# Kernel optimization log

Hardware: AMD Instinct MI355X
Metric: run time of the kernel (lower is better)

## Reference

```python
import jax, jax.numpy as jnp
import numpy as np

N = 100000
IN_C = 256
HID = 128


def setup_inputs() -> dict:
    key = jax.random.key(0)
    ks = jax.random.split(key, 8)
    x = jax.random.normal(ks[0], (N, IN_C), dtype=jnp.float32)
    edge_index = jax.random.randint(ks[1], (2, 1600000), 0, N, dtype=jnp.int64)
    # GCNConv: lin (bias=False) + separate additive bias
    W1 = jax.random.normal(ks[2], (IN_C, HID), dtype=jnp.float32) / np.sqrt(IN_C)
    b1 = jnp.zeros((HID,), dtype=jnp.float32)
    W2 = jax.random.normal(ks[3], (HID, HID // 2), dtype=jnp.float32) / np.sqrt(HID)
    b2 = jnp.zeros((HID // 2,), dtype=jnp.float32)
    Wfc = jax.random.normal(ks[4], (HID // 2, 2), dtype=jnp.float32) / np.sqrt(HID // 2)
    bfc = jnp.zeros((2,), dtype=jnp.float32)
    return {"x": x, "edge_index": edge_index, "W1": W1, "b1": b1,
            "W2": W2, "b2": b2, "Wfc": Wfc, "bfc": bfc}


def _gcn_norm(edge_index, n):
    # add self-loops, symmetric normalization (PyG gcn_norm defaults)
    loop = jnp.arange(n, dtype=edge_index.dtype)
    src = jnp.concatenate([edge_index[0], loop])
    dst = jnp.concatenate([edge_index[1], loop])
    deg = jax.ops.segment_sum(jnp.ones_like(src, dtype=jnp.float32), dst,
                              num_segments=n)
    dinv = jnp.where(deg > 0, jax.lax.rsqrt(deg), 0.0)
    norm = dinv[src] * dinv[dst]  # [E + N]
    return src, dst, norm


def _gcn_conv(x, W, b, src, dst, norm, n):
    h = x @ W                       # [N, out] dense transform first
    msg = h[src] * norm[:, None]    # irregular gather, [E+N, out]
    out = jax.ops.segment_sum(msg, dst, num_segments=n)  # scatter-add
    return out + b


def reference(x, edge_index, W1, b1, W2, b2, Wfc, bfc):
    n = x.shape[0]
    src, dst, norm = _gcn_norm(edge_index, n)
    h = jax.nn.relu(_gcn_conv(x, W1, b1, src, dst, norm, n))
    # dropout is identity in eval mode
    h = jax.nn.relu(_gcn_conv(h, W2, b2, src, dst, norm, n))
    logits = h @ Wfc + bfc  # [N, 2]
    return jax.nn.log_softmax(logits, axis=1)
```

## Files before the change

kernel.cpp:

```cpp
#include <hip/hip_runtime.h>
#include <math.h>

#define IN_C 256
#define HID 128
#define H2  64
#define CAP 64
#define NBK 391
#define BSLAB 8192

typedef __attribute__((ext_vector_type(8))) short bf16x8;
typedef __attribute__((ext_vector_type(4))) float f32x4;

__device__ __forceinline__ unsigned short f2bf(float f) {
  union { float f; unsigned int u; } v; v.f = f;
  unsigned int r = v.u + 0x7FFFu + ((v.u >> 16) & 1u);
  return (unsigned short)(r >> 16);
}
__device__ __forceinline__ float bf_lo(unsigned int u) {
  union { unsigned int u; float f; } v; v.u = u << 16; return v.f;
}
__device__ __forceinline__ float bf_hi(unsigned int u) {
  union { unsigned int u; float f; } v; v.u = u & 0xffff0000u; return v.f;
}
__device__ __forceinline__ unsigned int pack_bf(float lo, float hi) {
  return (unsigned int)f2bf(lo) | ((unsigned int)f2bf(hi) << 16);
}
__device__ __forceinline__ void add8(float* a, uint4 u) {
  a[0] += bf_lo(u.x); a[1] += bf_hi(u.x);
  a[2] += bf_lo(u.y); a[3] += bf_hi(u.y);
  a[4] += bf_lo(u.z); a[5] += bf_hi(u.z);
  a[6] += bf_lo(u.w); a[7] += bf_hi(u.w);
}

__global__ void wcast_kernel(const float* __restrict__ W, unsigned short* __restrict__ Wt,
                             int K, int N) {
  int idx = blockIdx.x * 256 + threadIdx.x;
  if (idx < K * N) {
    int nn = idx / K, kk = idx % K;
    Wt[idx] = f2bf(W[kk * N + nn]);
  }
}

__global__ __launch_bounds__(256) void scatter_kernel(
    const int* __restrict__ src, const int* __restrict__ dstA, int E,
    int* __restrict__ bucketFill , unsigned int* __restrict__ packed) {
  __shared__ int cnt[NBK];
  __shared__ int base[NBK];
  int tid = threadIdx.x;
  for (int i = tid; i < NBK; i += 256) cnt[i] = 0;
  __syncthreads();
  int e0 = blockIdx.x * 2048;
  int bk[8], ls[8]; unsigned int sv[8]; bool ok[8];
#pragma unroll
  for (int j = 0; j < 8; ++j) {
    int e = e0 + j * 256 + tid;
    ok[j] = e < E;
    int d = ok[j] ? dstA[e] : 0;
    int s = ok[j] ? src[e] : 0;
    bk[j] = d >> 8;
    sv[j] = ((unsigned int)s << 8) | (unsigned int)(d & 255);
    ls[j] = ok[j] ? atomicAdd(&cnt[bk[j]], 1) : 0;
  }
  __syncthreads();
  for (int i = tid; i < NBK; i += 256)
    base[i] = cnt[i] ? atomicAdd(&bucketFill[i * 16], cnt[i]) : 0;
  __syncthreads();
#pragma unroll
  for (int j = 0; j < 8; ++j)
    if (ok[j]) {
      int pos = base[bk[j]] + ls[j];
      if (pos < BSLAB) packed[(size_t)bk[j] * BSLAB + pos] = sv[j];
    }
}

__global__ __launch_bounds__(256) void bucket_csr_kernel(
    const unsigned int* __restrict__ packed, const int* __restrict__ bucketFill,
    int* __restrict__ fill, float* __restrict__ dinv, int* __restrict__ col, int n) {
  __shared__ int lcnt[256];
  int b = blockIdx.x;
  int t = threadIdx.x;
  lcnt[t] = 0;
  __syncthreads();
  int m = bucketFill[b * 16];
  if (m > BSLAB) m = BSLAB;
  const unsigned int* pp = packed + (size_t)b * BSLAB;
  int node0 = b * 256;
  for (int i = t; i < m; i += 256) {
    unsigned int p = pp[i];
    int lo = p & 255;
    int slot = atomicAdd(&lcnt[lo], 1);
    if (slot < CAP) col[(size_t)(node0 + lo) * CAP + slot] = (int)(p >> 8);
  }
  __syncthreads();
  int node = node0 + t;
  if (node < n) {
    int c = lcnt[t];
    fill[node] = c;
    dinv[node] = rsqrtf((float)(c + 1));
  }
}

template <int K, int N, int BM, int WM, int WN, bool A_BF16, bool SCALE>
__device__ __forceinline__ void gemm_body(const void* __restrict__ Av,
                                          const unsigned short* __restrict__ Bt,
                                          const float* __restrict__ dinv,
                                          unsigned short* __restrict__ C, int M,
                                          int bidx, short* As, short* Bs) {
  constexpr int WTM = BM / WM;
  constexpr int WTN = N / WN;
  constexpr int MB = WTM / 16, NB = WTN / 16;
  constexpr int ACH = BM * 4 / 256;
  constexpr int BCH = N * 4 / 256;

  int tid = threadIdx.x;
  int lane = tid & 63, wid = tid >> 6;
  int ln15 = lane & 15, kg = lane >> 4;
  int wm = wid / WN, wn = wid % WN;
  int row0 = bidx * BM;

  f32x4 acc[MB][NB];
#pragma unroll
  for (int i = 0; i < MB; ++i)
#pragma unroll
    for (int j = 0; j < NB; ++j) acc[i][j] = (f32x4)0.0f;

  for (int k0 = 0; k0 < K; k0 += 32) {
#pragma unroll
    for (int p = 0; p < ACH; ++p) {
      int c = p * 256 + tid;
      int row = c >> 2, kc = c & 3;
      int grow = row0 + row;
      if (A_BF16) {
        const unsigned short* Ab = (const unsigned short*)Av;
        uint4 v = make_uint4(0, 0, 0, 0);
        if (grow < M) v = *reinterpret_cast<const uint4*>(&Ab[(size_t)grow * K + k0 + kc * 8]);
        *reinterpret_cast<uint4*>(&As[row * 40 + kc * 8]) = v;
      } else {
        const float* A = (const float*)Av;
        float4 v0 = make_float4(0.f, 0.f, 0.f, 0.f), v1 = v0;
        if (grow < M) {
          const float4* ap = reinterpret_cast<const float4*>(&A[(size_t)grow * K + k0 + kc * 8]);
          v0 = ap[0]; v1 = ap[1];
        }
        bf16x8 w;
        w[0] = (short)f2bf(v0.x); w[1] = (short)f2bf(v0.y);
        w[2] = (short)f2bf(v0.z); w[3] = (short)f2bf(v0.w);
        w[4] = (short)f2bf(v1.x); w[5] = (short)f2bf(v1.y);
        w[6] = (short)f2bf(v1.z); w[7] = (short)f2bf(v1.w);
        *reinterpret_cast<bf16x8*>(&As[row * 40 + kc * 8]) = w;
      }
    }
#pragma unroll
    for (int p = 0; p < BCH; ++p) {
      int c = p * 256 + tid;
      int nrow = c >> 2, kc = c & 3;
      *reinterpret_cast<uint4*>(&Bs[nrow * 40 + kc * 8]) =
          *reinterpret_cast<const uint4*>(&Bt[(size_t)nrow * K + k0 + kc * 8]);
    }
    __syncthreads();
    bf16x8 af[MB], bfr[NB];
#pragma unroll
    for (int mb = 0; mb < MB; ++mb)
      af[mb] = *reinterpret_cast<const bf16x8*>(&As[(wm * WTM + mb * 16 + ln15) * 40 + kg * 8]);
#pragma unroll
    for (int nb = 0; nb < NB; ++nb)
      bfr[nb] = *reinterpret_cast<const bf16x8*>(&Bs[(wn * WTN + nb * 16 + ln15) * 40 + kg * 8]);
#pragma unroll
    for (int mb = 0; mb < MB; ++mb)
#pragma unroll
      for (int nb = 0; nb < NB; ++nb)
        acc[mb][nb] = __builtin_amdgcn_mfma_f32_16x16x32_bf16(af[mb], bfr[nb], acc[mb][nb], 0, 0, 0);
    __syncthreads();
  }
#pragma unroll
  for (int mb = 0; mb < MB; ++mb)
#pragma unroll
    for (int nb = 0; nb < NB; ++nb) {
      int gcol = wn * WTN + nb * 16 + ln15;
#pragma unroll
      for (int q = 0; q < 4; ++q) {
        int grow = row0 + wm * WTM + mb * 16 + kg * 4 + q;
        if (grow < M) {
          float v = acc[mb][nb][q];
          if (SCALE) v *= dinv[grow];
          C[(size_t)grow * N + gcol] = f2bf(v);
        }
      }
    }
}

__global__ __launch_bounds__(256) void gemm1_kernel(const float* __restrict__ A,
                                                    const unsigned short* __restrict__ Bt,
                                                    const float* __restrict__ dinv,
                                                    unsigned short* __restrict__ C, int M) {
  __shared__ short smem[(64 + HID) * 40];
  gemm_body<IN_C, HID, 64, 2, 2, false, true>(A, Bt, dinv, C, M, blockIdx.x,
                                              smem, smem + 64 * 40);
}

__global__ __launch_bounds__(256) void gemm2_kernel(const unsigned short* __restrict__ A,
                                                    const unsigned short* __restrict__ Bt,
                                                    unsigned short* __restrict__ C, int M) {
  __shared__ short smem[(64 + H2) * 40];
  gemm_body<HID, H2, 64, 2, 2, true, false>(A, Bt, nullptr, C, M, blockIdx.x,
                                            smem, smem + 64 * 40);
}

__global__ __launch_bounds__(256) void agg1_kernel(const uint4* __restrict__ hs4,
    const int* __restrict__ fill, const int* __restrict__ col,
    const float* __restrict__ dinv, const float* __restrict__ bias,
    uint4* __restrict__ outb, int n) {
  int sub = threadIdx.x >> 4, l = threadIdx.x & 15;
  int i = blockIdx.x * 16 + sub;
  if (i >= n) return;
  float di = dinv[i];
  int degi = fill[i];
  int cnt = degi > CAP ? CAP : degi;
  const int* cp = col + (size_t)i * CAP;
  float a[8];
  uint4 us = hs4[(size_t)i * 16 + l];
  a[0] = bf_lo(us.x); a[1] = bf_hi(us.x);
  a[2] = bf_lo(us.y); a[3] = bf_hi(us.y);
  a[4] = bf_lo(us.z); a[5] = bf_hi(us.z);
  a[6] = bf_lo(us.w); a[7] = bf_hi(us.w);
  int k = 0;
  for (; k + 7 < cnt; k += 8) {
    int c[8]; uint4 u[8];
#pragma unroll
    for (int j = 0; j < 8; ++j) c[j] = cp[k + j];
#pragma unroll
    for (int j = 0; j < 8; ++j) u[j] = hs4[(size_t)c[j] * 16 + l];
#pragma unroll
    for (int j = 0; j < 8; ++j) add8(a, u[j]);
  }
  for (; k + 3 < cnt; k += 4) {
    int c[4]; uint4 u[4];
#pragma unroll
    for (int j = 0; j < 4; ++j) c[j] = cp[k + j];
#pragma unroll
    for (int j = 0; j < 4; ++j) u[j] = hs4[(size_t)c[j] * 16 + l];
#pragma unroll
    for (int j = 0; j < 4; ++j) add8(a, u[j]);
  }
  for (; k < cnt; ++k) add8(a, hs4[(size_t)cp[k] * 16 + l]);
  float4 bA = reinterpret_cast<const float4*>(bias)[2 * l];
  float4 bB = reinterpret_cast<const float4*>(bias)[2 * l + 1];
  float r0 = di * fmaxf(di * a[0] + bA.x, 0.f);
  float r1 = di * fmaxf(di * a[1] + bA.y, 0.f);
  float r2 = di * fmaxf(di * a[2] + bA.z, 0.f);
  float r3 = di * fmaxf(di * a[3] + bA.w, 0.f);
  float r4 = di * fmaxf(di * a[4] + bB.x, 0.f);
  float r5 = di * fmaxf(di * a[5] + bB.y, 0.f);
  float r6 = di * fmaxf(di * a[6] + bB.z, 0.f);
  float r7 = di * fmaxf(di * a[7] + bB.w, 0.f);
  uint4 o;
  o.x = pack_bf(r0, r1); o.y = pack_bf(r2, r3);
  o.z = pack_bf(r4, r5); o.w = pack_bf(r6, r7);
  outb[(size_t)i * 16 + l] = o;
}

__global__ __launch_bounds__(256) void agg2fc_kernel(const uint4* __restrict__ hs4,
    const int* __restrict__ fill, const int* __restrict__ col,
    const float* __restrict__ dinv, const float* __restrict__ bias,
    const float* __restrict__ Wfc, const float* __restrict__ bfc,
    float* __restrict__ out, int n) {
  int sub = threadIdx.x >> 3, l = threadIdx.x & 7;
  int i = blockIdx.x * 32 + sub;
  if (i >= n) return;
  float di = dinv[i];
  int degi = fill[i];
  int cnt = degi > CAP ? CAP : degi;
  const int* cp = col + (size_t)i * CAP;
  float a[8];
  uint4 us = hs4[(size_t)i * 8 + l];
  a[0] = bf_lo(us.x); a[1] = bf_hi(us.x);
  a[2] = bf_lo(us.y); a[3] = bf_hi(us.y);
  a[4] = bf_lo(us.z); a[5] = bf_hi(us.z);
  a[6] = bf_lo(us.w); a[7] = bf_hi(us.w);
  int k = 0;
  for (; k + 7 < cnt; k += 8) {
    int c[8]; uint4 u[8];
#pragma unroll
    for (int j = 0; j < 8; ++j) c[j] = cp[k + j];
#pragma unroll
    for (int j = 0; j < 8; ++j) u[j] = hs4[(size_t)c[j] * 8 + l];
#pragma unroll
    for (int j = 0; j < 8; ++j) add8(a, u[j]);
  }
  for (; k + 3 < cnt; k += 4) {
    int c[4]; uint4 u[4];
#pragma unroll
    for (int j = 0; j < 4; ++j) c[j] = cp[k + j];
#pragma unroll
    for (int j = 0; j < 4; ++j) u[j] = hs4[(size_t)c[j] * 8 + l];
#pragma unroll
    for (int j = 0; j < 4; ++j) add8(a, u[j]);
  }
  for (; k < cnt; ++k) add8(a, hs4[(size_t)cp[k] * 8 + l]);
  float4 bA = reinterpret_cast<const float4*>(bias)[2 * l];
  float4 bB = reinterpret_cast<const float4*>(bias)[2 * l + 1];
  float r[8];
  r[0] = fmaxf(di * a[0] + bA.x, 0.f);
  r[1] = fmaxf(di * a[1] + bA.y, 0.f);
  r[2] = fmaxf(di * a[2] + bA.z, 0.f);
  r[3] = fmaxf(di * a[3] + bA.w, 0.f);
  r[4] = fmaxf(di * a[4] + bB.x, 0.f);
  r[5] = fmaxf(di * a[5] + bB.y, 0.f);
  r[6] = fmaxf(di * a[6] + bB.z, 0.f);
  r[7] = fmaxf(di * a[7] + bB.w, 0.f);
  float p0 = 0.f, p1 = 0.f;
#pragma unroll
  for (int s = 0; s < 4; ++s) {
    float4 w = reinterpret_cast<const float4*>(Wfc)[4 * l + s];
    p0 += r[2 * s] * w.x + r[2 * s + 1] * w.z;
    p1 += r[2 * s] * w.y + r[2 * s + 1] * w.w;
  }
#pragma unroll
  for (int off = 4; off; off >>= 1) {
    p0 += __shfl_xor(p0, off, 8);
    p1 += __shfl_xor(p1, off, 8);
  }
  if (l == 0) {
    float l0 = p0 + bfc[0], l1 = p1 + bfc[1];
    float m = fmaxf(l0, l1);
    float lse = m + logf(expf(l0 - m) + expf(l1 - m));
    float2 o; o.x = l0 - lse; o.y = l1 - lse;
    reinterpret_cast<float2*>(out)[i] = o;
  }
}

extern "C" void kernel_launch(void* const* d_in, const int* in_sizes, int n_in,
                              void* d_out, int out_size, void* d_ws, size_t ws_size,
                              hipStream_t stream) {
  const float* x   = (const float*)d_in[0];
  const int*   ei  = (const int*)d_in[1];
  const float* W1  = (const float*)d_in[2];
  const float* b1  = (const float*)d_in[3];
  const float* W2  = (const float*)d_in[4];
  const float* b2  = (const float*)d_in[5];
  const float* Wfc = (const float*)d_in[6];
  const float* bfc = (const float*)d_in[7];
  float* out = (float*)d_out;

  int n = in_sizes[0] / IN_C;
  int E = in_sizes[1] / 2;
  const int* src = ei;
  const int* dst = ei + E;

  char* ws = (char*)d_ws;
  size_t off = 0;
  auto alloc = [&](size_t bytes) {
    void* p = ws + off;
    off = (off + bytes + 255) & ~(size_t)255;
    return p;
  };
  int*   fill       = (int*)alloc((size_t)n * 4);
  float* dinv       = (float*)alloc((size_t)n * 4);
  int*   bucketFill = (int*)alloc((size_t)NBK * 16 * 4);
  unsigned int* packed = (unsigned int*)alloc((size_t)NBK * BSLAB * 4);
  int*   col    = (int*)alloc((size_t)n * CAP * 4);
  unsigned short* h1lin = (unsigned short*)alloc((size_t)n * HID * 2);
  unsigned short* h1    = (unsigned short*)alloc((size_t)n * HID * 2);
  unsigned short* h2lin = (unsigned short*)alloc((size_t)n * H2 * 2);
  unsigned short* W1T   = (unsigned short*)alloc((size_t)IN_C * HID * 2);
  unsigned short* W2T   = (unsigned short*)alloc((size_t)HID * H2 * 2);

  hipMemsetAsync(bucketFill, 0, (size_t)NBK * 16 * 4, stream);
  wcast_kernel<<<(IN_C * HID + 255) / 256, 256, 0, stream>>>(W1, W1T, IN_C, HID);
  wcast_kernel<<<(HID * H2 + 255) / 256, 256, 0, stream>>>(W2, W2T, HID, H2);

  scatter_kernel<<<(E + 2047) / 2048, 256, 0, stream>>>(src, dst, E, bucketFill, packed);
  bucket_csr_kernel<<<NBK, 256, 0, stream>>>(packed, bucketFill, fill, dinv, col, n);

  gemm1_kernel<<<(n + 63) / 64, 256, 0, stream>>>(x, W1T, dinv, h1lin, n);
  agg1_kernel<<<(n + 15) / 16, 256, 0, stream>>>((const uint4*)h1lin, fill, col, dinv, b1, (uint4*)h1, n);
  gemm2_kernel<<<(n + 63) / 64, 256, 0, stream>>>(h1, W2T, h2lin, n);
  agg2fc_kernel<<<(n + 31) / 32, 256, 0, stream>>>((const uint4*)h2lin, fill, col, dinv, b2, Wfc, bfc, out, n);
}
```

Before: 198.8 us.

## Double-buffer GEMM shared-memory tiles with register prefetch of next K-slab

Restructures the GEMM main loop into a two-stage software pipeline. Global loads for the next K-slab go into registers before the MFMA work on the current LDS buffer, then get stored into the alternate LDS buffer, which removes one barrier per step. This doubles LDS use per block and raises register pressure. ACH is hardcoded to one chunk per thread, which holds for BM=64.

```diff
diff --git a/kernel.cpp b/kernel.cpp
--- a/kernel.cpp
+++ b/kernel.cpp
@@ -109,14 +109,15 @@
   constexpr int WTM = BM / WM;
   constexpr int WTN = N / WN;
   constexpr int MB = WTM / 16, NB = WTN / 16;
-  constexpr int ACH = BM * 4 / 256;
-  constexpr int BCH = N * 4 / 256;
+  constexpr int BCH = N / 64;
+  constexpr int NSTEP = K / 32;
 
   int tid = threadIdx.x;
   int lane = tid & 63, wid = tid >> 6;
   int ln15 = lane & 15, kg = lane >> 4;
   int wm = wid / WN, wn = wid % WN;
   int row0 = bidx * BM;
+  int arow = tid >> 2, akc = tid & 3;
 
   f32x4 acc[MB][NB];
 #pragma unroll
@@ -124,53 +125,75 @@
 #pragma unroll
     for (int j = 0; j < NB; ++j) acc[i][j] = (f32x4)0.0f;
 
-  for (int k0 = 0; k0 < K; k0 += 32) {
-#pragma unroll
-    for (int p = 0; p < ACH; ++p) {
-      int c = p * 256 + tid;
-      int row = c >> 2, kc = c & 3;
-      int grow = row0 + row;
-      if (A_BF16) {
-        const unsigned short* Ab = (const unsigned short*)Av;
-        uint4 v = make_uint4(0, 0, 0, 0);
-        if (grow < M) v = *reinterpret_cast<const uint4*>(&Ab[(size_t)grow * K + k0 + kc * 8]);
-        *reinterpret_cast<uint4*>(&As[row * 40 + kc * 8]) = v;
-      } else {
-        const float* A = (const float*)Av;
-        float4 v0 = make_float4(0.f, 0.f, 0.f, 0.f), v1 = v0;
-        if (grow < M) {
-          const float4* ap = reinterpret_cast<const float4*>(&A[(size_t)grow * K + k0 + kc * 8]);
-          v0 = ap[0]; v1 = ap[1];
-        }
-        bf16x8 w;
-        w[0] = (short)f2bf(v0.x); w[1] = (short)f2bf(v0.y);
-        w[2] = (short)f2bf(v0.z); w[3] = (short)f2bf(v0.w);
-        w[4] = (short)f2bf(v1.x); w[5] = (short)f2bf(v1.y);
-        w[6] = (short)f2bf(v1.z); w[7] = (short)f2bf(v1.w);
-        *reinterpret_cast<bf16x8*>(&As[row * 40 + kc * 8]) = w;
+  float4 av0, av1; uint4 avb;
+  uint4 bvb[BCH];
+
+  auto loadTile = [&](int k0) {
+    int grow = row0 + arow;
+    if (A_BF16) {
+      const unsigned short* Ab = (const unsigned short*)Av;
+      avb = make_uint4(0, 0, 0, 0);
+      if (grow < M) avb = *reinterpret_cast<const uint4*>(&Ab[(size_t)grow * K + k0 + akc * 8]);
+    } else {
+      const float* A = (const float*)Av;
+      av0 = make_float4(0.f, 0.f, 0.f, 0.f); av1 = av0;
+      if (grow < M) {
+        const float4* ap = reinterpret_cast<const float4*>(&A[(size_t)grow * K + k0 + akc * 8]);
+        av0 = ap[0]; av1 = ap[1];
       }
     }
 #pragma unroll
     for (int p = 0; p < BCH; ++p) {
       int c = p * 256 + tid;
       int nrow = c >> 2, kc = c & 3;
-      *reinterpret_cast<uint4*>(&Bs[nrow * 40 + kc * 8]) =
-          *reinterpret_cast<const uint4*>(&Bt[(size_t)nrow * K + k0 + kc * 8]);
-    }
-    __syncthreads();
+      bvb[p] = *reinterpret_cast<const uint4*>(&Bt[(size_t)nrow * K + k0 + kc * 8]);
+    }
+  };
+  auto storeTile = [&](int buf) {
+    short* Aw = As + buf * BM * 40;
+    short* Bw = Bs + buf * N * 40;
+    if (A_BF16) {
+      *reinterpret_cast<uint4*>(&Aw[arow * 40 + akc * 8]) = avb;
+    } else {
+      bf16x8 w;
+      w[0] = (short)f2bf(av0.x); w[1] = (short)f2bf(av0.y);
+      w[2] = (short)f2bf(av0.z); w[3] = (short)f2bf(av0.w);
+      w[4] = (short)f2bf(av1.x); w[5] = (short)f2bf(av1.y);
+      w[6] = (short)f2bf(av1.z); w[7] = (short)f2bf(av1.w);
+      *reinterpret_cast<bf16x8*>(&Aw[arow * 40 + akc * 8]) = w;
+    }
+#pragma unroll
+    for (int p = 0; p < BCH; ++p) {
+      int c = p * 256 + tid;
+      int nrow = c >> 2, kc = c & 3;
+      *reinterpret_cast<uint4*>(&Bw[nrow * 40 + kc * 8]) = bvb[p];
+    }
+  };
+
+  loadTile(0);
+  storeTile(0);
+  __syncthreads();
+  int cur = 0;
+  for (int s = 0; s < NSTEP; ++s) {
+    bool hasNext = (s + 1 < NSTEP);
+    if (hasNext) loadTile((s + 1) * 32);
+    const short* Ar = As + cur * BM * 40;
+    const short* Br = Bs + cur * N * 40;
     bf16x8 af[MB], bfr[NB];
 #pragma unroll
     for (int mb = 0; mb < MB; ++mb)
-      af[mb] = *reinterpret_cast<const bf16x8*>(&As[(wm * WTM + mb * 16 + ln15) * 40 + kg * 8]);
+      af[mb] = *reinterpret_cast<const bf16x8*>(&Ar[(wm * WTM + mb * 16 + ln15) * 40 + kg * 8]);
 #pragma unroll
     for (int nb = 0; nb < NB; ++nb)
-      bfr[nb] = *reinterpret_cast<const bf16x8*>(&Bs[(wn * WTN + nb * 16 + ln15) * 40 + kg * 8]);
+      bfr[nb] = *reinterpret_cast<const bf16x8*>(&Br[(wn * WTN + nb * 16 + ln15) * 40 + kg * 8]);
 #pragma unroll
     for (int mb = 0; mb < MB; ++mb)
 #pragma unroll
       for (int nb = 0; nb < NB; ++nb)
         acc[mb][nb] = __builtin_amdgcn_mfma_f32_16x16x32_bf16(af[mb], bfr[nb], acc[mb][nb], 0, 0, 0);
+    if (hasNext) storeTile(cur ^ 1);
     __syncthreads();
+    cur ^= 1;
   }
 #pragma unroll
   for (int mb = 0; mb < MB; ++mb)
@@ -193,17 +216,17 @@
                                                     const unsigned short* __restrict__ Bt,
                                                     const float* __restrict__ dinv,
                                                     unsigned short* __restrict__ C, int M) {
-  __shared__ short smem[(64 + HID) * 40];
+  __shared__ short smem[2 * (64 + HID) * 40];
   gemm_body<IN_C, HID, 64, 2, 2, false, true>(A, Bt, dinv, C, M, blockIdx.x,
-                                              smem, smem + 64 * 40);
+                                              smem, smem + 2 * 64 * 40);
 }
 
 __global__ __launch_bounds__(256) void gemm2_kernel(const unsigned short* __restrict__ A,
                                                     const unsigned short* __restrict__ Bt,
                                                     unsigned short* __restrict__ C, int M) {
-  __shared__ short smem[(64 + H2) * 40];
+  __shared__ short smem[2 * (64 + H2) * 40];
   gemm_body<HID, H2, 64, 2, 2, true, false>(A, Bt, nullptr, C, M, blockIdx.x,
-                                            smem, smem + 64 * 40);
+                                            smem, smem + 2 * 64 * 40);
 }
 
 __global__ __launch_bounds__(256) void agg1_kernel(const uint4* __restrict__ hs4,
```

After: 197.8 us. Within noise of the previous version (-0.5%).

## Restructure GEMM to stage full A tile once and stream B from registers

Applied to the files above, without the earlier changes.

The K-loop GEMM, which staged A and B tiles in LDS with two barriers per 32-wide K step, is replaced by a single-barrier version. It loads the entire 64xK A tile into LDS at once and has each wave read its B fragments straight from global memory into registers, in phases of up to four K-steps. This removes the per-step barrier and the LDS round trip for B, at the cost of more LDS per block (about 33KB for gemm1), which may lower occupancy, and more register pressure from the held B fragments.

```diff
diff --git a/kernel.cpp b/kernel.cpp
--- a/kernel.cpp
+++ b/kernel.cpp
@@ -100,86 +100,100 @@
   }
 }
 
-template <int K, int N, int BM, int WM, int WN, bool A_BF16, bool SCALE>
-__device__ __forceinline__ void gemm_body(const void* __restrict__ Av,
-                                          const unsigned short* __restrict__ Bt,
-                                          const float* __restrict__ dinv,
-                                          unsigned short* __restrict__ C, int M,
-                                          int bidx, short* As, short* Bs) {
-  constexpr int WTM = BM / WM;
-  constexpr int WTN = N / WN;
-  constexpr int MB = WTM / 16, NB = WTN / 16;
-  constexpr int ACH = BM * 4 / 256;
-  constexpr int BCH = N * 4 / 256;
+template <int K, int N, bool A_BF16, bool SCALE>
+__device__ __forceinline__ void gemm_onebar_body(const void* __restrict__ Av,
+                                                 const unsigned short* __restrict__ Bt,
+                                                 const float* __restrict__ dinv,
+                                                 unsigned short* __restrict__ C, int M,
+                                                 int bidx, short* As) {
+  constexpr int BM = 64;
+  constexpr int PITCH = K + 8;
+  constexpr int NB = N / 32;
+  constexpr int KS = K / 32;
+  constexpr int PH = (KS < 4) ? KS : 4;
+  constexpr int CH = BM * K / (256 * 8);
 
   int tid = threadIdx.x;
   int lane = tid & 63, wid = tid >> 6;
   int ln15 = lane & 15, kg = lane >> 4;
-  int wm = wid / WN, wn = wid % WN;
+  int wm = wid >> 1, wn = wid & 1;
   int row0 = bidx * BM;
 
-  f32x4 acc[MB][NB];
-#pragma unroll
-  for (int i = 0; i < MB; ++i)
+  if (A_BF16) {
+    const unsigned short* Ab = (const unsigned short*)Av;
+#pragma unroll
+    for (int c = 0; c < CH; ++c) {
+      int idx = c * 2048 + tid * 8;
+      int row = idx / K, colk = idx % K;
+      uint4 v = make_uint4(0, 0, 0, 0);
+      int grow = row0 + row;
+      if (grow < M) v = *reinterpret_cast<const uint4*>(&Ab[(size_t)grow * K + colk]);
+      *reinterpret_cast<uint4*>(&As[row * PITCH + colk]) = v;
+    }
+  } else {
+    const float* A = (const float*)Av;
+#pragma unroll
+    for (int c = 0; c < CH; ++c) {
+      int idx = c * 2048 + tid * 8;
+      int row = idx / K, colk = idx % K;
+      float4 v0 = make_float4(0.f, 0.f, 0.f, 0.f), v1 = v0;
+      int grow = row0 + row;
+      if (grow < M) {
+        const float4* ap = reinterpret_cast<const float4*>(&A[(size_t)grow * K + colk]);
+        v0 = ap[0]; v1 = ap[1];
+      }
+      bf16x8 w;
+      w[0] = (short)f2bf(v0.x); w[1] = (short)f2bf(v0.y);
+      w[2] = (short)f2bf(v0.z); w[3] = (short)f2bf(v0.w);
+      w[4] = (short)f2bf(v1.x); w[5] = (short)f2bf(v1.y);
+      w[6] = (short)f2bf(v1.z); w[7] = (short)f2bf(v1.w);
+      *reinterpret_cast<bf16x8*>(&As[row * PITCH + colk]) = w;
+    }
+  }
+
+  bf16x8 breg[NB][PH];
+  auto loadB = [&](int ks0) {
+#pragma unroll
+    for (int nb = 0; nb < NB; ++nb)
+#pragma unroll
+      for (int p = 0; p < PH; ++p)
+        breg[nb][p] = *reinterpret_cast<const bf16x8*>(
+            &Bt[(size_t)(wn * (N / 2) + nb * 16 + ln15) * K + (ks0 + p) * 32 + kg * 8]);
+  };
+  loadB(0);
+  __syncthreads();
+
+  f32x4 acc[2][NB];
+#pragma unroll
+  for (int i = 0; i < 2; ++i)
 #pragma unroll
     for (int j = 0; j < NB; ++j) acc[i][j] = (f32x4)0.0f;
 
-  for (int k0 = 0; k0 < K; k0 += 32) {
-#pragma unroll
-    for (int p = 0; p < ACH; ++p) {
-      int c = p * 256 + tid;
-      int row = c >> 2, kc = c & 3;
-      int grow = row0 + row;
-      if (A_BF16) {
-        const unsigned short* Ab = (const unsigned short*)Av;
-        uint4 v = make_uint4(0, 0, 0, 0);
-        if (grow < M) v = *reinterpret_cast<const uint4*>(&Ab[(size_t)grow * K + k0 + kc * 8]);
-        *reinterpret_cast<uint4*>(&As[row * 40 + kc * 8]) = v;
-      } else {
-        const float* A = (const float*)Av;
-        float4 v0 = make_float4(0.f, 0.f, 0.f, 0.f), v1 = v0;
-        if (grow < M) {
-          const float4* ap = reinterpret_cast<const float4*>(&A[(size_t)grow * K + k0 + kc * 8]);
-          v0 = ap[0]; v1 = ap[1];
-        }
-        bf16x8 w;
-        w[0] = (short)f2bf(v0.x); w[1] = (short)f2bf(v0.y);
-        w[2] = (short)f2bf(v0.z); w[3] = (short)f2bf(v0.w);
-        w[4] = (short)f2bf(v1.x); w[5] = (short)f2bf(v1.y);
-        w[6] = (short)f2bf(v1.z); w[7] = (short)f2bf(v1.w);
-        *reinterpret_cast<bf16x8*>(&As[row * 40 + kc * 8]) = w;
+#pragma unroll
+  for (int ph = 0; ph < KS / PH; ++ph) {
+    if (ph > 0) loadB(ph * PH);
+#pragma unroll
+    for (int p = 0; p < PH; ++p) {
+      int ks = ph * PH + p;
+      bf16x8 af0 = *reinterpret_cast<const bf16x8*>(
+          &As[(wm * 32 + ln15) * PITCH + ks * 32 + kg * 8]);
+      bf16x8 af1 = *reinterpret_cast<const bf16x8*>(
+          &As[(wm * 32 + 16 + ln15) * PITCH + ks * 32 + kg * 8]);
+#pragma unroll
+      for (int nb = 0; nb < NB; ++nb) {
+        acc[0][nb] = __builtin_amdgcn_mfma_f32_16x16x32_bf16(af0, breg[nb][p], acc[0][nb], 0, 0, 0);
+        acc[1][nb] = __builtin_amdgcn_mfma_f32_16x16x32_bf16(af1, breg[nb][p], acc[1][nb], 0, 0, 0);
       }
     }
-#pragma unroll
-    for (int p = 0; p < BCH; ++p) {
-      int c = p * 256 + tid;
-      int nrow = c >> 2, kc = c & 3;
-      *reinterpret_cast<uint4*>(&Bs[nrow * 40 + kc * 8]) =
-          *reinterpret_cast<const uint4*>(&Bt[(size_t)nrow * K + k0 + kc * 8]);
-    }
-    __syncthreads();
-    bf16x8 af[MB], bfr[NB];
-#pragma unroll
-    for (int mb = 0; mb < MB; ++mb)
-      af[mb] = *reinterpret_cast<const bf16x8*>(&As[(wm * WTM + mb * 16 + ln15) * 40 + kg * 8]);
-#pragma unroll
-    for (int nb = 0; nb < NB; ++nb)
-      bfr[nb] = *reinterpret_cast<const bf16x8*>(&Bs[(wn * WTN + nb * 16 + ln15) * 40 + kg * 8]);
-#pragma unroll
-    for (int mb = 0; mb < MB; ++mb)
-#pragma unroll
-      for (int nb = 0; nb < NB; ++nb)
-        acc[mb][nb] = __builtin_amdgcn_mfma_f32_16x16x32_bf16(af[mb], bfr[nb], acc[mb][nb], 0, 0, 0);
-    __syncthreads();
-  }
-#pragma unroll
-  for (int mb = 0; mb < MB; ++mb)
+  }
+#pragma unroll
+  for (int mb = 0; mb < 2; ++mb)
 #pragma unroll
     for (int nb = 0; nb < NB; ++nb) {
-      int gcol = wn * WTN + nb * 16 + ln15;
+      int gcol = wn * (N / 2) + nb * 16 + ln15;
 #pragma unroll
       for (int q = 0; q < 4; ++q) {
-        int grow = row0 + wm * WTM + mb * 16 + kg * 4 + q;
+        int grow = row0 + wm * 32 + mb * 16 + kg * 4 + q;
         if (grow < M) {
           float v = acc[mb][nb][q];
           if (SCALE) v *= dinv[grow];
@@ -193,17 +207,15 @@
                                                     const unsigned short* __restrict__ Bt,
                                                     const float* __restrict__ dinv,
                                                     unsigned short* __restrict__ C, int M) {
-  __shared__ short smem[(64 + HID) * 40];
-  gemm_body<IN_C, HID, 64, 2, 2, false, true>(A, Bt, dinv, C, M, blockIdx.x,
-                                              smem, smem + 64 * 40);
+  __shared__ short smem[64 * (IN_C + 8)];
+  gemm_onebar_body<IN_C, HID, false, true>(A, Bt, dinv, C, M, blockIdx.x, smem);
 }
 
 __global__ __launch_bounds__(256) void gemm2_kernel(const unsigned short* __restrict__ A,
                                                     const unsigned short* __restrict__ Bt,
                                                     unsigned short* __restrict__ C, int M) {
-  __shared__ short smem[(64 + H2) * 40];
-  gemm_body<HID, H2, 64, 2, 2, true, false>(A, Bt, nullptr, C, M, blockIdx.x,
-                                            smem, smem + 64 * 40);
+  __shared__ short smem[64 * (HID + 8)];
+  gemm_onebar_body<HID, H2, true, false>(A, Bt, nullptr, C, M, blockIdx.x, smem);
 }
 
 __global__ __launch_bounds__(256) void agg1_kernel(const uint4* __restrict__ hs4,
```

After: 227.6 us. 1.15x slower.
